# Performance work log

Hardware: AMD Instinct MI355X
Metric: run time of the kernel (lower is better)

## Reference

```python
import jax, jax.numpy as jnp
import numpy as np

NUM_HEADS = 8
EPS = 1e-3

N_TOKENS = 32768
DIM = 256
N_WIN = 128
WIN = N_TOKENS // N_WIN  # 256 tokens per window


def setup_inputs() -> dict:
    key = jax.random.key(0)
    ks = jax.random.split(key, 4)
    x = jax.random.normal(ks[0], (N_TOKENS, DIM), dtype=jnp.float32)
    # torch nn.Linear weights are [out_features, in_features]
    w_qkv = jax.random.normal(ks[1], (3 * DIM, DIM), dtype=jnp.float32) * (DIM ** -0.5)
    w_proj = jax.random.normal(ks[2], (DIM, DIM), dtype=jnp.float32) * (DIM ** -0.5)
    b_proj = jnp.zeros((DIM,), dtype=jnp.float32)
    batch_win_inds = (jnp.arange(N_TOKENS) // WIN).astype(jnp.int64)
    offsets = (jnp.arange(N_WIN) * WIN).astype(jnp.int64)
    counts = jnp.full((N_WIN,), WIN, dtype=jnp.int64)
    return {"x": x, "w_qkv": w_qkv, "w_proj": w_proj, "b_proj": b_proj,
            "offsets": offsets, "counts": counts, "batch_win_inds": batch_win_inds}


def reference(x, w_qkv, w_proj, b_proj, offsets, counts, batch_win_inds):
    N, C = x.shape
    H = NUM_HEADS
    hd = C // H
    W = counts.shape[0]  # number of windows (static)

    qkv = x @ w_qkv.T                      # [N, 3C]
    q, k, v = jnp.split(qkv, 3, axis=-1)   # each [N, C]
    q = jax.nn.relu(q.reshape(N, H, hd))   # [N, H, hd]
    k = jax.nn.relu(k.reshape(N, H, hd))
    v = v.reshape(N, H, hd)

    seg = batch_win_inds.astype(jnp.int32)
    # per-window KV state: kv[w] = sum_{i in w} k_i^T v_i   -> [W, H, hd, hd]
    kv = jax.ops.segment_sum(jnp.einsum('nhc,nhd->nhcd', k, v), seg, num_segments=W)
    # per-window key sum for normalizer                      -> [W, H, hd]
    s = jax.ops.segment_sum(k, seg, num_segments=W)

    y = jnp.einsum('nhc,nhcd->nhd', q, kv[seg])              # [N, H, hd]
    z = jnp.sum(s[seg] * q, axis=-1, keepdims=True)          # [N, H, 1]
    y = y / (z + EPS)

    y = y.reshape(N, C) @ w_proj.T + b_proj                  # [N, C]
    return y
```

## Files before the change

kernel.cpp:

```cpp
#include <hip/hip_runtime.h>

typedef __bf16 bf16_t;
typedef bf16_t bf16x8 __attribute__((ext_vector_type(8)));
typedef bf16_t bf16x4 __attribute__((ext_vector_type(4)));
typedef float f32x4 __attribute__((ext_vector_type(4)));

#define M_TOK 32768
#define NWIN 128
#define WIN  256
#define NX_ELEMS 8388608
#define NQ_ELEMS 196608

typedef __attribute__((address_space(3))) void* as3p;
typedef const __attribute__((address_space(1))) void* as1p;

__device__ __forceinline__ void gll16(const void* g, void* l) {
    __builtin_amdgcn_global_load_lds((as1p)g, (as3p)l, 16, 0, 0);
}

__global__ __launch_bounds__(256) void xwconv(
    const float* __restrict__ x, const float* __restrict__ wq,
    const float* __restrict__ wp,
    bf16_t* __restrict__ xb, bf16_t* __restrict__ wqb, bf16_t* __restrict__ wpb)
{
    int i4 = (blockIdx.x * 256 + threadIdx.x) * 4;
    const float* s; bf16_t* dst; int idx;
    if (i4 < NX_ELEMS)                  { s = x;  dst = xb;  idx = i4; }
    else if (i4 < NX_ELEMS + NQ_ELEMS)  { s = wq; dst = wqb; idx = i4 - NX_ELEMS; }
    else                                { s = wp; dst = wpb; idx = i4 - NX_ELEMS - NQ_ELEMS; }
    f32x4 v = *(const f32x4*)(s + idx);
    bf16x4 o;
    o[0] = (bf16_t)v[0]; o[1] = (bf16_t)v[1]; o[2] = (bf16_t)v[2]; o[3] = (bf16_t)v[3];
    *(bf16x4*)(dst + idx) = o;
}

template<int QBLK>
__global__ __launch_bounds__(256) void gemm1t(
    const bf16_t* __restrict__ Xb,
    const bf16_t* __restrict__ Wb,
    bf16_t* __restrict__ Qg,
    bf16_t* __restrict__ KTg,
    bf16_t* __restrict__ VTg)
{
    __shared__ bf16_t As[2][128][32];
    __shared__ bf16_t Bs[2][128][32];

    const int tid = threadIdx.x;
    const int lane = tid & 63;
    const int wv = tid >> 6;
    const int wm = wv >> 1, wn = wv & 1;
    const int id = blockIdx.x;
    int m0, n0;
    if (QBLK) { m0 = (id >> 1) * 128; n0 = (id & 1) * 128; }
    else      { m0 = (id >> 2) * 128; n0 = 256 + (id & 3) * 128; }
    const int r = lane & 15, q = lane >> 4;
    const int srow = lane >> 2;

    f32x4 acc[4][4] = {};

    for (int kc = 0; kc < 256; kc += 64) {
#pragma unroll
        for (int p = 0; p < 2; ++p)
#pragma unroll
            for (int g = 0; g < 2; ++g) {
                const int rb = wv * 32 + g * 16;
                gll16(Xb + (size_t)(m0 + rb + srow) * 256 + kc + p * 32 + (lane & 3) * 8,
                      &As[p][rb][0]);
                gll16(Wb + (size_t)(n0 + rb + srow) * 256 + kc + p * 32 + (lane & 3) * 8,
                      &Bs[p][rb][0]);
            }
        __syncthreads();

#pragma unroll
        for (int kk = 0; kk < 64; kk += 32) {
            const int pA = kk >> 5;
            bf16x8 a[4], b[4];
#pragma unroll
            for (int i = 0; i < 4; ++i)
                a[i] = *(const bf16x8*)&As[pA][wm * 64 + i * 16 + r][q * 8];
#pragma unroll
            for (int j = 0; j < 4; ++j)
                b[j] = *(const bf16x8*)&Bs[pA][wn * 64 + j * 16 + r][q * 8];
            if (QBLK) {
#pragma unroll
                for (int i = 0; i < 4; ++i)
#pragma unroll
                    for (int j = 0; j < 4; ++j)
                        acc[i][j] = __builtin_amdgcn_mfma_f32_16x16x32_bf16(b[j], a[i], acc[i][j], 0, 0, 0);
            } else {
#pragma unroll
                for (int i = 0; i < 4; ++i)
#pragma unroll
                    for (int j = 0; j < 4; ++j)
                        acc[i][j] = __builtin_amdgcn_mfma_f32_16x16x32_bf16(a[i], b[j], acc[i][j], 0, 0, 0);
            }
        }
        __syncthreads();
    }

    if (QBLK) {
#pragma unroll
        for (int i = 0; i < 4; ++i) {
            const int rowg = m0 + wm * 64 + i * 16 + r;
#pragma unroll
            for (int j = 0; j < 4; ++j) {
                const int nb = n0 + wn * 64 + j * 16 + q * 4;
                const int hq = nb >> 5, d = nb & 31;
                bf16x4 o;
#pragma unroll
                for (int reg = 0; reg < 4; ++reg)
                    o[reg] = (bf16_t)fmaxf(acc[i][j][reg], 0.0f);
                *(bf16x4*)&Qg[((size_t)hq * M_TOK + rowg) * 32 + d] = o;
            }
        }
    } else {
        const bool isK = (n0 < 512);
        bf16_t* base = isK ? KTg : VTg;
#pragma unroll
        for (int i = 0; i < 4; ++i) {
            const int tok0 = m0 + wm * 64 + i * 16 + q * 4;
#pragma unroll
            for (int j = 0; j < 4; ++j) {
                const int nb = n0 + wn * 64 + j * 16 + r;
                const int hh = (nb >> 5) & 7;
                const int c  = nb & 31;
                bf16x4 o;
#pragma unroll
                for (int reg = 0; reg < 4; ++reg) {
                    float v = acc[i][j][reg];
                    if (isK) v = fmaxf(v, 0.0f);
                    o[reg] = (bf16_t)v;
                }
                *(bf16x4*)&base[((size_t)hh * 32 + c) * M_TOK + tok0] = o;
            }
        }
    }
}

__global__ __launch_bounds__(256) void gemm2_proj(
    const bf16_t* __restrict__ Y,
    const bf16_t* __restrict__ Wb,
    const float* __restrict__ bias,
    float* __restrict__ Out)
{
    __shared__ bf16_t As[2][64][32];
    __shared__ bf16_t Bs[2][128][32];

    const int tid = threadIdx.x;
    const int lane = tid & 63;
    const int wv = tid >> 6;
    const int id = blockIdx.x;
    const int sg = id / 16, wsub = id % 16;
    const int m0 = (sg * 8 + (wsub & 7)) * 64;
    const int n0 = (wsub >> 3) * 128;
    const int r = lane & 15, q = lane >> 4;
    const int srow = lane >> 2;

    f32x4 acc[4][2] = {};

    for (int kc = 0; kc < 256; kc += 64) {
#pragma unroll
        for (int p = 0; p < 2; ++p)
            gll16(Y + (size_t)(m0 + wv * 16 + srow) * 256 + kc + p * 32 + (lane & 3) * 8,
                  &As[p][wv * 16][0]);
#pragma unroll
        for (int p = 0; p < 2; ++p)
#pragma unroll
            for (int g = 0; g < 2; ++g)
                gll16(Wb + (size_t)(n0 + wv * 32 + g * 16 + srow) * 256 + kc + p * 32 + (lane & 3) * 8,
                      &Bs[p][wv * 32 + g * 16][0]);
        __syncthreads();

#pragma unroll
        for (int kk = 0; kk < 64; kk += 32) {
            const int pB = kk >> 5;
            bf16x8 a[4], b[2];
#pragma unroll
            for (int i = 0; i < 4; ++i)
                a[i] = *(const bf16x8*)&As[pB][i * 16 + r][q * 8];
#pragma unroll
            for (int j = 0; j < 2; ++j)
                b[j] = *(const bf16x8*)&Bs[pB][wv * 32 + j * 16 + r][q * 8];
#pragma unroll
            for (int i = 0; i < 4; ++i)
#pragma unroll
                for (int j = 0; j < 2; ++j)
                    acc[i][j] = __builtin_amdgcn_mfma_f32_16x16x32_bf16(b[j], a[i], acc[i][j], 0, 0, 0);
        }
        __syncthreads();
    }

#pragma unroll
    for (int i = 0; i < 4; ++i) {
        const int rowg = m0 + i * 16 + r;
#pragma unroll
        for (int j = 0; j < 2; ++j) {
            const int nb = n0 + wv * 32 + j * 16 + q * 4;
            f32x4 bi = *(const f32x4*)(bias + nb);
            f32x4 o;
#pragma unroll
            for (int reg = 0; reg < 4; ++reg) o[reg] = acc[i][j][reg] + bi[reg];
            *(f32x4*)&Out[(size_t)rowg * 256 + nb] = o;
        }
    }
}

__global__ __launch_bounds__(256) void kvy_kernel(
    const bf16_t* __restrict__ Qg,
    const bf16_t* __restrict__ KTg,
    const bf16_t* __restrict__ VTg,
    const int* __restrict__ offsets,
    const int* __restrict__ counts,
    bf16_t* __restrict__ Y)
{
    const int w = blockIdx.x;
    const int h = blockIdx.y;
    const int is64 = (counts[1] == 0) ? 1 : 0;
    const int off = offsets[w << is64];
    const int tid = threadIdx.x;
    const int lane = tid & 63;
    const int wv = tid >> 6;
    const int r = lane & 15, q = lane >> 4;

    __shared__ __align__(16) bf16_t KVT[32 * 40];
    __shared__ float sbuf[32];
    __shared__ float zinv[WIN];

    {
        const int i = wv >> 1, j = wv & 1;
        bf16x8 ones;
#pragma unroll
        for (int u = 0; u < 8; ++u) ones[u] = (bf16_t)1.0f;
        f32x4 acc = {}, accs = {};
        const bf16_t* kr = KTg + ((size_t)h * 32 + i * 16 + r) * M_TOK + off + q * 8;
        const bf16_t* vr = VTg + ((size_t)h * 32 + j * 16 + r) * M_TOK + off + q * 8;
#pragma unroll
        for (int ch = 0; ch < 8; ++ch) {
            bf16x8 af = *(const bf16x8*)(kr + ch * 32);
            bf16x8 bf_ = *(const bf16x8*)(vr + ch * 32);
            acc  = __builtin_amdgcn_mfma_f32_16x16x32_bf16(af, bf_, acc, 0, 0, 0);
            accs = __builtin_amdgcn_mfma_f32_16x16x32_bf16(af, ones, accs, 0, 0, 0);
        }
        bf16x4 kv4;
#pragma unroll
        for (int reg = 0; reg < 4; ++reg) kv4[reg] = (bf16_t)acc[reg];
        *(bf16x4*)(&KVT[(j * 16 + r) * 40 + i * 16 + q * 4]) = kv4;
        if (j == 0 && r == 0) {
#pragma unroll
            for (int reg = 0; reg < 4; ++reg)
                sbuf[i * 16 + q * 4 + reg] = accs[reg];
        }
    }
    __syncthreads();

    {
        const int t = tid;
        const bf16_t* qp = Qg + ((size_t)h * M_TOK + off + t) * 32;
        float z = 0.f;
#pragma unroll
        for (int u = 0; u < 4; ++u) {
            bf16x8 qq = *(const bf16x8*)(qp + u * 8);
#pragma unroll
            for (int jj = 0; jj < 8; ++jj) z += (float)qq[jj] * sbuf[u * 8 + jj];
        }
        zinv[t] = 1.0f / (z + 1e-3f);
    }
    __syncthreads();

    {
        bf16x8 b0 = *(const bf16x8*)(&KVT[(r) * 40 + q * 8]);
        bf16x8 b1 = *(const bf16x8*)(&KVT[(16 + r) * 40 + q * 8]);
#pragma unroll
        for (int u = 0; u < 4; ++u) {
            const int mi = wv * 4 + u;
            const bf16_t* ap = Qg + ((size_t)h * M_TOK + off + mi * 16 + r) * 32 + q * 8;
            bf16x8 af = *(const bf16x8*)ap;
            f32x4 acc0 = {}, acc1 = {};
            acc0 = __builtin_amdgcn_mfma_f32_16x16x32_bf16(b0, af, acc0, 0, 0, 0);
            acc1 = __builtin_amdgcn_mfma_f32_16x16x32_bf16(b1, af, acc1, 0, 0, 0);
            const int tkn = mi * 16 + r;
            const float zi = zinv[tkn];
            bf16_t* yp = Y + (size_t)(off + tkn) * 256 + h * 32;
            bf16x4 o0, o1;
#pragma unroll
            for (int reg = 0; reg < 4; ++reg) {
                o0[reg] = (bf16_t)(acc0[reg] * zi);
                o1[reg] = (bf16_t)(acc1[reg] * zi);
            }
            *(bf16x4*)(yp + q * 4) = o0;
            *(bf16x4*)(yp + 16 + q * 4) = o1;
        }
    }
}

extern "C" void kernel_launch(void* const* d_in, const int* in_sizes, int n_in,
                              void* d_out, int out_size, void* d_ws, size_t ws_size,
                              hipStream_t stream) {
    const float* x      = (const float*)d_in[0];
    const float* w_qkv  = (const float*)d_in[1];
    const float* w_proj = (const float*)d_in[2];
    const float* b_proj = (const float*)d_in[3];
    const int*   offs   = (const int*)d_in[4];
    const int*   cnts   = (const int*)d_in[5];

    char* ws = (char*)d_ws;
    bf16_t* Xb  = (bf16_t*)ws;
    bf16_t* Qg  = (bf16_t*)(ws + 16777216);
    bf16_t* KTg = (bf16_t*)(ws + 33554432);
    bf16_t* VTg = (bf16_t*)(ws + 50331648);
    bf16_t* Wqb = (bf16_t*)(ws + 67108864);
    bf16_t* Wpb = (bf16_t*)(ws + 67502080);
    bf16_t* Y   = Xb;
    float*  out = (float*)d_out;

    xwconv<<<8448, 256, 0, stream>>>(x, w_qkv, w_proj, Xb, Wqb, Wpb);

    gemm1t<1><<<512, 256, 0, stream>>>(Xb, Wqb, Qg, KTg, VTg);
    gemm1t<0><<<1024, 256, 0, stream>>>(Xb, Wqb, Qg, KTg, VTg);

    kvy_kernel<<<dim3(NWIN, 8), 256, 0, stream>>>(Qg, KTg, VTg, offs, cnts, Y);

    gemm2_proj<<<1024, 256, 0, stream>>>(Y, Wpb, b_proj, out);
}
```

Baseline: 152.2 us.

## Fuse fp32-to-bf16 conversion of x into the Q projection GEMM

The separate pass that converted all of x to bf16 is removed. The Q GEMM now loads fp32 x directly, converts it in registers, stores it to LDS, and has the n0==0 blocks also write the bf16 copy for the later K/V GEMM. The weight conversion keeps its own small kernel. The kvy kernel now issues all K/V fragment loads before its MFMA loop to raise memory-level parallelism, at the cost of more registers; the Q GEMM's A operand also loses its async global-to-LDS loads.

```diff
diff --git a/kernel.cpp b/kernel.cpp
--- a/kernel.cpp
+++ b/kernel.cpp
@@ -8,7 +8,6 @@
 #define M_TOK 32768
 #define NWIN 128
 #define WIN  256
-#define NX_ELEMS 8388608
 #define NQ_ELEMS 196608
 
 typedef __attribute__((address_space(3))) void* as3p;
@@ -18,29 +17,32 @@
     __builtin_amdgcn_global_load_lds((as1p)g, (as3p)l, 16, 0, 0);
 }
 
-__global__ __launch_bounds__(256) void xwconv(
-    const float* __restrict__ x, const float* __restrict__ wq,
-    const float* __restrict__ wp,
-    bf16_t* __restrict__ xb, bf16_t* __restrict__ wqb, bf16_t* __restrict__ wpb)
+__device__ __forceinline__ bf16x8 cvt8(f32x4 a, f32x4 b) {
+    bf16x8 o;
+    o[0] = (bf16_t)a[0]; o[1] = (bf16_t)a[1]; o[2] = (bf16_t)a[2]; o[3] = (bf16_t)a[3];
+    o[4] = (bf16_t)b[0]; o[5] = (bf16_t)b[1]; o[6] = (bf16_t)b[2]; o[7] = (bf16_t)b[3];
+    return o;
+}
+
+__global__ __launch_bounds__(256) void wconv(
+    const float* __restrict__ wq, const float* __restrict__ wp,
+    bf16_t* __restrict__ wqb, bf16_t* __restrict__ wpb)
 {
     int i4 = (blockIdx.x * 256 + threadIdx.x) * 4;
     const float* s; bf16_t* dst; int idx;
-    if (i4 < NX_ELEMS)                  { s = x;  dst = xb;  idx = i4; }
-    else if (i4 < NX_ELEMS + NQ_ELEMS)  { s = wq; dst = wqb; idx = i4 - NX_ELEMS; }
-    else                                { s = wp; dst = wpb; idx = i4 - NX_ELEMS - NQ_ELEMS; }
+    if (i4 < NQ_ELEMS) { s = wq; dst = wqb; idx = i4; }
+    else               { s = wp; dst = wpb; idx = i4 - NQ_ELEMS; }
     f32x4 v = *(const f32x4*)(s + idx);
     bf16x4 o;
     o[0] = (bf16_t)v[0]; o[1] = (bf16_t)v[1]; o[2] = (bf16_t)v[2]; o[3] = (bf16_t)v[3];
     *(bf16x4*)(dst + idx) = o;
 }
 
-template<int QBLK>
-__global__ __launch_bounds__(256) void gemm1t(
-    const bf16_t* __restrict__ Xb,
+__global__ __launch_bounds__(256) void gemm1_q(
+    const float* __restrict__ X,
     const bf16_t* __restrict__ Wb,
-    bf16_t* __restrict__ Qg,
-    bf16_t* __restrict__ KTg,
-    bf16_t* __restrict__ VTg)
+    bf16_t* __restrict__ Xb,
+    bf16_t* __restrict__ Qg)
 {
     __shared__ bf16_t As[2][128][32];
     __shared__ bf16_t Bs[2][128][32];
@@ -50,9 +52,88 @@
     const int wv = tid >> 6;
     const int wm = wv >> 1, wn = wv & 1;
     const int id = blockIdx.x;
-    int m0, n0;
-    if (QBLK) { m0 = (id >> 1) * 128; n0 = (id & 1) * 128; }
-    else      { m0 = (id >> 2) * 128; n0 = 256 + (id & 3) * 128; }
+    const int m0 = (id >> 1) * 128, n0 = (id & 1) * 128;
+    const int r = lane & 15, q = lane >> 4;
+    const int srow = lane >> 2;
+    const bool wxb = (n0 == 0);
+
+    const int arow = tid >> 3;
+    const int acol = (tid & 7) * 8;
+
+    f32x4 acc[4][4] = {};
+
+    for (int kc = 0; kc < 256; kc += 64) {
+#pragma unroll
+        for (int p = 0; p < 4; ++p) {
+            const int row = p * 32 + arow;
+            const float* xp = X + (size_t)(m0 + row) * 256 + kc + acol;
+            f32x4 lo = *(const f32x4*)xp;
+            f32x4 hi = *(const f32x4*)(xp + 4);
+            bf16x8 cv = cvt8(lo, hi);
+            *(bf16x8*)&As[acol >> 5][row][acol & 31] = cv;
+            if (wxb) *(bf16x8*)&Xb[(size_t)(m0 + row) * 256 + kc + acol] = cv;
+        }
+#pragma unroll
+        for (int p = 0; p < 2; ++p)
+#pragma unroll
+            for (int g = 0; g < 2; ++g) {
+                const int rb = wv * 32 + g * 16;
+                gll16(Wb + (size_t)(n0 + rb + srow) * 256 + kc + p * 32 + (lane & 3) * 8,
+                      &Bs[p][rb][0]);
+            }
+        __syncthreads();
+
+#pragma unroll
+        for (int kk = 0; kk < 64; kk += 32) {
+            const int pA = kk >> 5;
+            bf16x8 a[4], b[4];
+#pragma unroll
+            for (int i = 0; i < 4; ++i)
+                a[i] = *(const bf16x8*)&As[pA][wm * 64 + i * 16 + r][q * 8];
+#pragma unroll
+            for (int j = 0; j < 4; ++j)
+                b[j] = *(const bf16x8*)&Bs[pA][wn * 64 + j * 16 + r][q * 8];
+#pragma unroll
+            for (int i = 0; i < 4; ++i)
+#pragma unroll
+                for (int j = 0; j < 4; ++j)
+                    acc[i][j] = __builtin_amdgcn_mfma_f32_16x16x32_bf16(b[j], a[i], acc[i][j], 0, 0, 0);
+        }
+        __syncthreads();
+    }
+
+#pragma unroll
+    for (int i = 0; i < 4; ++i) {
+        const int rowg = m0 + wm * 64 + i * 16 + r;
+#pragma unroll
+        for (int j = 0; j < 4; ++j) {
+            const int nb = n0 + wn * 64 + j * 16 + q * 4;
+            const int hq = nb >> 5, d = nb & 31;
+            bf16x4 o;
+#pragma unroll
+            for (int reg = 0; reg < 4; ++reg)
+                o[reg] = (bf16_t)fmaxf(acc[i][j][reg], 0.0f);
+            *(bf16x4*)&Qg[((size_t)hq * M_TOK + rowg) * 32 + d] = o;
+        }
+    }
+}
+
+__global__ __launch_bounds__(256) void gemm1_kv(
+    const bf16_t* __restrict__ Xb,
+    const bf16_t* __restrict__ Wb,
+    bf16_t* __restrict__ KTg,
+    bf16_t* __restrict__ VTg)
+{
+    __shared__ bf16_t As[2][128][32];
+    __shared__ bf16_t Bs[2][128][32];
+
+    const int tid = threadIdx.x;
+    const int lane = tid & 63;
+    const int wv = tid >> 6;
+    const int wm = wv >> 1, wn = wv & 1;
+    const int id = blockIdx.x;
+    const int m0 = (id >> 2) * 128;
+    const int n0 = 256 + (id & 3) * 128;
     const int r = lane & 15, q = lane >> 4;
     const int srow = lane >> 2;
 
@@ -81,58 +162,33 @@
 #pragma unroll
             for (int j = 0; j < 4; ++j)
                 b[j] = *(const bf16x8*)&Bs[pA][wn * 64 + j * 16 + r][q * 8];
-            if (QBLK) {
-#pragma unroll
-                for (int i = 0; i < 4; ++i)
-#pragma unroll
-                    for (int j = 0; j < 4; ++j)
-                        acc[i][j] = __builtin_amdgcn_mfma_f32_16x16x32_bf16(b[j], a[i], acc[i][j], 0, 0, 0);
-            } else {
-#pragma unroll
-                for (int i = 0; i < 4; ++i)
-#pragma unroll
-                    for (int j = 0; j < 4; ++j)
-                        acc[i][j] = __builtin_amdgcn_mfma_f32_16x16x32_bf16(a[i], b[j], acc[i][j], 0, 0, 0);
+#pragma unroll
+            for (int i = 0; i < 4; ++i)
+#pragma unroll
+                for (int j = 0; j < 4; ++j)
+                    acc[i][j] = __builtin_amdgcn_mfma_f32_16x16x32_bf16(a[i], b[j], acc[i][j], 0, 0, 0);
+        }
+        __syncthreads();
+    }
+
+    const bool isK = (n0 < 512);
+    bf16_t* base = isK ? KTg : VTg;
+#pragma unroll
+    for (int i = 0; i < 4; ++i) {
+        const int tok0 = m0 + wm * 64 + i * 16 + q * 4;
+#pragma unroll
+        for (int j = 0; j < 4; ++j) {
+            const int nb = n0 + wn * 64 + j * 16 + r;
+            const int hh = (nb >> 5) & 7;
+            const int c  = nb & 31;
+            bf16x4 o;
+#pragma unroll
+            for (int reg = 0; reg < 4; ++reg) {
+                float v = acc[i][j][reg];
+                if (isK) v = fmaxf(v, 0.0f);
+                o[reg] = (bf16_t)v;
             }
-        }
-        __syncthreads();
-    }
-
-    if (QBLK) {
-#pragma unroll
-        for (int i = 0; i < 4; ++i) {
-            const int rowg = m0 + wm * 64 + i * 16 + r;
-#pragma unroll
-            for (int j = 0; j < 4; ++j) {
-                const int nb = n0 + wn * 64 + j * 16 + q * 4;
-                const int hq = nb >> 5, d = nb & 31;
-                bf16x4 o;
-#pragma unroll
-                for (int reg = 0; reg < 4; ++reg)
-                    o[reg] = (bf16_t)fmaxf(acc[i][j][reg], 0.0f);
-                *(bf16x4*)&Qg[((size_t)hq * M_TOK + rowg) * 32 + d] = o;
-            }
-        }
-    } else {
-        const bool isK = (n0 < 512);
-        bf16_t* base = isK ? KTg : VTg;
-#pragma unroll
-        for (int i = 0; i < 4; ++i) {
-            const int tok0 = m0 + wm * 64 + i * 16 + q * 4;
-#pragma unroll
-            for (int j = 0; j < 4; ++j) {
-                const int nb = n0 + wn * 64 + j * 16 + r;
-                const int hh = (nb >> 5) & 7;
-                const int c  = nb & 31;
-                bf16x4 o;
-#pragma unroll
-                for (int reg = 0; reg < 4; ++reg) {
-                    float v = acc[i][j][reg];
-                    if (isK) v = fmaxf(v, 0.0f);
-                    o[reg] = (bf16_t)v;
-                }
-                *(bf16x4*)&base[((size_t)hh * 32 + c) * M_TOK + tok0] = o;
-            }
+            *(bf16x4*)&base[((size_t)hh * 32 + c) * M_TOK + tok0] = o;
         }
     }
 }
@@ -231,15 +287,19 @@
         bf16x8 ones;
 #pragma unroll
         for (int u = 0; u < 8; ++u) ones[u] = (bf16_t)1.0f;
-        f32x4 acc = {}, accs = {};
         const bf16_t* kr = KTg + ((size_t)h * 32 + i * 16 + r) * M_TOK + off + q * 8;
         const bf16_t* vr = VTg + ((size_t)h * 32 + j * 16 + r) * M_TOK + off + q * 8;
+        bf16x8 kfr[8], vfr[8];
 #pragma unroll
         for (int ch = 0; ch < 8; ++ch) {
-            bf16x8 af = *(const bf16x8*)(kr + ch * 32);
-            bf16x8 bf_ = *(const bf16x8*)(vr + ch * 32);
-            acc  = __builtin_amdgcn_mfma_f32_16x16x32_bf16(af, bf_, acc, 0, 0, 0);
-            accs = __builtin_amdgcn_mfma_f32_16x16x32_bf16(af, ones, accs, 0, 0, 0);
+            kfr[ch] = *(const bf16x8*)(kr + ch * 32);
+            vfr[ch] = *(const bf16x8*)(vr + ch * 32);
+        }
+        f32x4 acc = {}, accs = {};
+#pragma unroll
+        for (int ch = 0; ch < 8; ++ch) {
+            acc  = __builtin_amdgcn_mfma_f32_16x16x32_bf16(kfr[ch], vfr[ch], acc, 0, 0, 0);
+            accs = __builtin_amdgcn_mfma_f32_16x16x32_bf16(kfr[ch], ones, accs, 0, 0, 0);
         }
         bf16x4 kv4;
 #pragma unroll
@@ -313,10 +373,11 @@
     bf16_t* Y   = Xb;
     float*  out = (float*)d_out;
 
-    xwconv<<<8448, 256, 0, stream>>>(x, w_qkv, w_proj, Xb, Wqb, Wpb);
-
-    gemm1t<1><<<512, 256, 0, stream>>>(Xb, Wqb, Qg, KTg, VTg);
-    gemm1t<0><<<1024, 256, 0, stream>>>(Xb, Wqb, Qg, KTg, VTg);
+    wconv<<<256, 256, 0, stream>>>(w_qkv, w_proj, Wqb, Wpb);
+
+    gemm1_q<<<512, 256, 0, stream>>>(x, Wqb, Xb, Qg);
+
+    gemm1_kv<<<1024, 256, 0, stream>>>(Xb, Wqb, KTg, VTg);
 
     kvy_kernel<<<dim3(NWIN, 8), 256, 0, stream>>>(Qg, KTg, VTg, offs, cnts, Y);
 
```

Measured after the change: 159.7 us. 4.9% more time.
